# Optimization experiments

Measured on AMD Instinct MI355X. Metric: run time of the kernel, lower is better.

## Reference

```python
import jax, jax.numpy as jnp
import numpy as np

T, B, S = 64, 32, 128
E, Q, H = 512, 512, 256  # src_encoding_size, query_vec_size, hidden_dim


def setup_inputs() -> dict:
    key = jax.random.key(0)
    ks = jax.random.split(key, 9)
    return {
        "src_encodings": jax.random.normal(ks[0], (B, S, E), jnp.float32),
        "src_token_mask": jax.random.randint(ks[1], (B, S), 0, 2).astype(bool),
        "query_vec": jax.random.normal(ks[2], (T, B, Q), jnp.float32),
        # learned params (nn.Linear stores W as (out, in))
        "W_src": jax.random.normal(ks[3], (H, E), jnp.float32) * (1.0 / np.sqrt(E)),
        "b_src": jax.random.normal(ks[4], (H,), jnp.float32) * 0.01,
        "W_q": jax.random.normal(ks[5], (H, Q), jnp.float32) * (1.0 / np.sqrt(Q)),
        "b_q": jax.random.normal(ks[6], (H,), jnp.float32) * 0.01,
        "w2": jax.random.normal(ks[7], (H,), jnp.float32) * (1.0 / np.sqrt(H)),
        "b2": jax.random.normal(ks[8], (), jnp.float32) * 0.01,
    }


def reference(src_encodings, src_token_mask, query_vec, W_src, b_src, W_q, b_q, w2, b2):
    # src projection: (B,S,H); query projection: (T,B,H)
    src_proj = jnp.einsum('bse,he->bsh', src_encodings, W_src) + b_src
    q_proj = jnp.einsum('tbq,hq->tbh', query_vec, W_q) + b_q
    # broadcast add -> tanh: (T,B,S,H)
    h1 = jnp.tanh(src_proj[None, :, :, :] + q_proj[:, :, None, :])
    # hidden -> 1 reduction: (T,B,S)
    h2 = jnp.einsum('tbsh,h->tbs', h1, w2) + b2
    h2 = jnp.where(src_token_mask[None, :, :], -jnp.inf, h2)
    return jax.nn.softmax(h2, axis=-1)
```

## Files before the change

### kernel.cpp

```cpp
#include <hip/hip_runtime.h>
#include <hip/hip_bf16.h>
#include <math.h>


#define TANH_PRESCALE 2.8853900817779268f
#define LOG2E        1.4426950408889634f

typedef __attribute__((ext_vector_type(8))) short short8;
typedef __attribute__((ext_vector_type(4))) float f32x4;

__device__ __forceinline__ float fast_exp2(float x) {
#if __has_builtin(__builtin_amdgcn_exp2f)
    return __builtin_amdgcn_exp2f(x);
#else
    return exp2f(x);
#endif
}
__device__ __forceinline__ float fast_rcp(float x) {
#if __has_builtin(__builtin_amdgcn_rcpf)
    return __builtin_amdgcn_rcpf(x);
#else
    return 1.0f / x;
#endif
}
__device__ __forceinline__ float hi_part(float x) {
    return __uint_as_float(__float_as_uint(x) & 0xffff0000u);
}
__device__ __forceinline__ unsigned pack2(float a, float b) {
    return __builtin_amdgcn_perm(__float_as_uint(b), __float_as_uint(a), 0x07060302u);
}

#define AHI 0
#define ALO 4608
#define WHI 9216
#define WLO 13824
#define LDS_USH 18432

__global__ __launch_bounds__(256) void proj_gemm(
    const float* __restrict__ src, const float* __restrict__ query,
    const float* __restrict__ Wsrc, const float* __restrict__ Wq,
    const float* __restrict__ b_src, const float* __restrict__ b_q,
    float* __restrict__ spq, float* __restrict__ qp)
{
    const int lin = blockIdx.x;
    const int g   = lin & 7;
    const int r   = lin >> 3;
    const int nb  = r & 3;
    const int bx  = (r >> 2) * 8 + g;

    const bool isSrc = bx < 64;
    const int mrow0 = (isSrc ? bx : bx - 64) * 64;
    const float* __restrict__ A    = isSrc ? src  : query;
    const float* __restrict__ W    = isSrc ? Wsrc : Wq;
    const float* __restrict__ bias = isSrc ? b_src : b_q;

    __shared__ unsigned short LS[LDS_USH];

    const int tid  = threadIdx.x;
    const int lane = tid & 63;
    const int wv   = tid >> 6;
    const int wm   = wv & 1, wn = wv >> 1;
    const int l15  = lane & 15;
    const int q4   = lane >> 4;

    const int srow = tid >> 3;
    const int sc8  = tid & 7;

    f32x4 acc[2][2];
    #pragma unroll
    for (int i = 0; i < 2; ++i)
        #pragma unroll
        for (int j = 0; j < 2; ++j) acc[i][j] = (f32x4){0.f, 0.f, 0.f, 0.f};

    const float* Ab = A + (size_t)mrow0 * 512 + sc8 * 8;
    const float* Wb = W + (size_t)(nb * 64) * 512 + sc8 * 8;

    for (int kt = 0; kt < 512; kt += 64) {
        __syncthreads();
        #pragma unroll
        for (int p = 0; p < 2; ++p) {
            const int row = srow + 32 * p;
            const float* gp = Ab + (size_t)row * 512 + kt;
            float4 v0 = *(const float4*)gp, v1 = *(const float4*)(gp + 4);
            uint4 h; uint4 l;
            h.x = pack2(v0.x, v0.y);  h.y = pack2(v0.z, v0.w);
            h.z = pack2(v1.x, v1.y);  h.w = pack2(v1.z, v1.w);
            l.x = pack2(v0.x - hi_part(v0.x), v0.y - hi_part(v0.y));
            l.y = pack2(v0.z - hi_part(v0.z), v0.w - hi_part(v0.w));
            l.z = pack2(v1.x - hi_part(v1.x), v1.y - hi_part(v1.y));
            l.w = pack2(v1.z - hi_part(v1.z), v1.w - hi_part(v1.w));
            *(uint4*)&LS[AHI + row * 72 + sc8 * 8] = h;
            *(uint4*)&LS[ALO + row * 72 + sc8 * 8] = l;
        }
        #pragma unroll
        for (int p = 0; p < 2; ++p) {
            const int row = srow + 32 * p;
            const float* gp = Wb + (size_t)row * 512 + kt;
            float4 v0 = *(const float4*)gp, v1 = *(const float4*)(gp + 4);
            uint4 h; uint4 l;
            h.x = pack2(v0.x, v0.y);  h.y = pack2(v0.z, v0.w);
            h.z = pack2(v1.x, v1.y);  h.w = pack2(v1.z, v1.w);
            l.x = pack2(v0.x - hi_part(v0.x), v0.y - hi_part(v0.y));
            l.y = pack2(v0.z - hi_part(v0.z), v0.w - hi_part(v0.w));
            l.z = pack2(v1.x - hi_part(v1.x), v1.y - hi_part(v1.y));
            l.w = pack2(v1.z - hi_part(v1.z), v1.w - hi_part(v1.w));
            *(uint4*)&LS[WHI + row * 72 + sc8 * 8] = h;
            *(uint4*)&LS[WLO + row * 72 + sc8 * 8] = l;
        }
        __syncthreads();

        #pragma unroll
        for (int pass = 0; pass < 3; ++pass) {
            const unsigned short* Ap = LS + (pass == 2 ? ALO : AHI);
            const unsigned short* Wp = LS + (pass == 1 ? WLO : WHI);
            #pragma unroll
            for (int kk = 0; kk < 2; ++kk) {
                const int off = (kk * 4 + q4) * 8;
                short8 a0 = *(const short8*)&Ap[(wm * 32 + l15)      * 72 + off];
                short8 a1 = *(const short8*)&Ap[(wm * 32 + 16 + l15) * 72 + off];
                short8 w0 = *(const short8*)&Wp[(wn * 32 + l15)      * 72 + off];
                short8 w1 = *(const short8*)&Wp[(wn * 32 + 16 + l15) * 72 + off];
                acc[0][0] = __builtin_amdgcn_mfma_f32_16x16x32_bf16(a0, w0, acc[0][0], 0, 0, 0);
                acc[0][1] = __builtin_amdgcn_mfma_f32_16x16x32_bf16(a0, w1, acc[0][1], 0, 0, 0);
                acc[1][0] = __builtin_amdgcn_mfma_f32_16x16x32_bf16(a1, w0, acc[1][0], 0, 0, 0);
                acc[1][1] = __builtin_amdgcn_mfma_f32_16x16x32_bf16(a1, w1, acc[1][1], 0, 0, 0);
            }
        }
    }

    float bl[2];
    #pragma unroll
    for (int ni = 0; ni < 2; ++ni)
        bl[ni] = bias[nb * 64 + wn * 32 + ni * 16 + l15];

    __syncthreads();
    float* E = (float*)LS;
    #pragma unroll
    for (int mi = 0; mi < 2; ++mi)
        #pragma unroll
        for (int ni = 0; ni < 2; ++ni) {
            const int m = wm * 32 + mi * 16 + q4 * 4;
            const int n = wn * 32 + ni * 16 + l15;
            #pragma unroll
            for (int rr = 0; rr < 4; ++rr)
                E[(m + rr) * 68 + n] = (acc[mi][ni][rr] + bl[ni]) * TANH_PRESCALE;
        }
    __syncthreads();

    if (isSrc) {
        const int nq = tid >> 4;
        #pragma unroll
        for (int j = 0; j < 4; ++j) {
            const int m = (tid & 15) + 16 * j;
            float4 v = *(const float4*)&E[m * 68 + nq * 4];
            *(float4*)(spq + (size_t)(nb * 16 + nq) * 16384
                           + (size_t)(mrow0 + m) * 4) = v;
        }
    } else {
        #pragma unroll
        for (int p = 0; p < 4; ++p) {
            const int idx = p * 256 + tid;
            const int m = idx >> 4, c4 = idx & 15;
            float4 v = *(const float4*)&E[m * 68 + c4 * 4];
            *(float4*)(qp + (size_t)(mrow0 + m) * 256 + nb * 64 + c4 * 4) = v;
        }
    }
}

__global__ __launch_bounds__(512) void attn_score(
    const float* __restrict__ spq, const float* __restrict__ qp,
    const float* __restrict__ w2, const int* __restrict__ mask,
    float* __restrict__ out)
{
    const int lin = blockIdx.x;
    const int gx  = lin & 7;
    const int rr  = lin >> 3;
    const int tz  = rr & 15;
    const int b   = (rr >> 4) * 8 + gx;

    const int tid = threadIdx.x;

    __shared__ float qp_s[4][256];
    __shared__ float w2_s[256];
    __shared__ float h2p[4][4][128];

    int mk0 = 0, mk1 = 0;
    if (tid < 256) {
        const int tl = tid >> 6, lane = tid & 63;
        const int t = tz * 4 + tl;
        *(float4*)&qp_s[tl][lane * 4] =
            *(const float4*)(qp + (size_t)(t * 32 + b) * 256 + lane * 4);
        mk0 = mask[b * 128 + lane];
        mk1 = mask[b * 128 + lane + 64];
    } else if (tid < 320) {
        const int i = tid - 256;
        *(float4*)&w2_s[i * 4] = *(const float4*)(w2 + i * 4);
    }
    __syncthreads();

    const int s = tid & 127;
    const int g4 = tid >> 7;
    const int hb = g4 * 64;
    const float* sq = spq + (size_t)(g4 * 16) * 16384 + (size_t)(b * 128 + s) * 4;

    float acc0 = 0.f, acc1 = 0.f, acc2 = 0.f, acc3 = 0.f;
    float4 s4 = *(const float4*)sq;
    #pragma unroll 4
    for (int hq = 0; hq < 16; ++hq) {
        float4 nxt;
        if (hq < 15) nxt = *(const float4*)(sq + (size_t)(hq + 1) * 16384);
        float4 w4 = *(const float4*)&w2_s[hb + hq * 4];
        float4 q0 = *(const float4*)&qp_s[0][hb + hq * 4];
        float4 q1 = *(const float4*)&qp_s[1][hb + hq * 4];
        float4 q2 = *(const float4*)&qp_s[2][hb + hq * 4];
        float4 q3 = *(const float4*)&qp_s[3][hb + hq * 4];
        #define PN_TERM(sj, wj, q0j, q1j, q2j, q3j)                              \
            { float r_;                                                          \
              r_ = fast_rcp(fast_exp2(sj + q0j) + 1.0f); acc0 = fmaf(wj, r_, acc0);\
              r_ = fast_rcp(fast_exp2(sj + q1j) + 1.0f); acc1 = fmaf(wj, r_, acc1);\
              r_ = fast_rcp(fast_exp2(sj + q2j) + 1.0f); acc2 = fmaf(wj, r_, acc2);\
              r_ = fast_rcp(fast_exp2(sj + q3j) + 1.0f); acc3 = fmaf(wj, r_, acc3); }
        PN_TERM(s4.x, w4.x, q0.x, q1.x, q2.x, q3.x)
        PN_TERM(s4.y, w4.y, q0.y, q1.y, q2.y, q3.y)
        PN_TERM(s4.z, w4.z, q0.z, q1.z, q2.z, q3.z)
        PN_TERM(s4.w, w4.w, q0.w, q1.w, q2.w, q3.w)
        #undef PN_TERM
        s4 = nxt;
    }
    h2p[g4][0][s] = acc0;
    h2p[g4][1][s] = acc1;
    h2p[g4][2][s] = acc2;
    h2p[g4][3][s] = acc3;
    __syncthreads();

    if (tid < 256) {
        const int wv = tid >> 6, lane = tid & 63;
        float v0 = -2.0f * (h2p[0][wv][lane] + h2p[1][wv][lane]
                          + h2p[2][wv][lane] + h2p[3][wv][lane]);
        float v1 = -2.0f * (h2p[0][wv][lane + 64] + h2p[1][wv][lane + 64]
                          + h2p[2][wv][lane + 64] + h2p[3][wv][lane + 64]);
        if (mk0) v0 = -__builtin_inff();
        if (mk1) v1 = -__builtin_inff();

        float mx = fmaxf(v0, v1);
        #pragma unroll
        for (int off = 32; off >= 1; off >>= 1) mx = fmaxf(mx, __shfl_xor(mx, off));
        float e0 = fast_exp2((v0 - mx) * LOG2E);
        float e1 = fast_exp2((v1 - mx) * LOG2E);
        float sum = e0 + e1;
        #pragma unroll
        for (int off = 32; off >= 1; off >>= 1) sum += __shfl_xor(sum, off);
        const float r_ = fast_rcp(sum);

        const size_t ob = (size_t)((tz * 4 + wv) * 32 + b) * 128;
        out[ob + lane]      = e0 * r_;
        out[ob + lane + 64] = e1 * r_;
    }
}

extern "C" void kernel_launch(void* const* d_in, const int* in_sizes, int n_in,
                              void* d_out, int out_size, void* d_ws, size_t ws_size,
                              hipStream_t stream) {
    const float* src   = (const float*)d_in[0];
    const int*   mask  = (const int*)  d_in[1];
    const float* query = (const float*)d_in[2];
    const float* W_src = (const float*)d_in[3];
    const float* b_src = (const float*)d_in[4];
    const float* W_q   = (const float*)d_in[5];
    const float* b_q   = (const float*)d_in[6];
    const float* w2    = (const float*)d_in[7];
    float* out = (float*)d_out;

    float* spq = (float*)d_ws;
    float* qp  = (float*)((char*)d_ws + (4u << 20));

    proj_gemm<<<384, 256, 0, stream>>>(src, query, W_src, W_q,
                                       b_src, b_q, spq, qp);
    attn_score<<<512, 512, 0, stream>>>(spq, qp, w2, mask, out);
}
```

Measured before the change: 102.2 us.

## Stage src projections through double-buffered LDS and simplify block index mapping

The attention-score kernel now prefetches the src-projection chunks from global memory into a double-buffered shared-memory tile and computes from that tile. Previously each thread streamed its own chunks straight from global memory. Both kernels also drop the XCD-aware block swizzle in favour of plain grid indexing, with proj_gemm launched on a 2D grid. The change adds two block barriers per stage and more LDS use. Removing the swizzle may also hurt L2 locality across the chiplets.

```diff
diff --git a/kernel.cpp b/kernel.cpp
--- a/kernel.cpp
+++ b/kernel.cpp
@@ -42,12 +42,8 @@
     const float* __restrict__ b_src, const float* __restrict__ b_q,
     float* __restrict__ spq, float* __restrict__ qp)
 {
-    const int lin = blockIdx.x;
-    const int g   = lin & 7;
-    const int r   = lin >> 3;
-    const int nb  = r & 3;
-    const int bx  = (r >> 2) * 8 + g;
-
+    const int bx = blockIdx.x;
+    const int nb = blockIdx.y;
     const bool isSrc = bx < 64;
     const int mrow0 = (isSrc ? bx : bx - 64) * 64;
     const float* __restrict__ A    = isSrc ? src  : query;
@@ -173,16 +169,15 @@
     float* __restrict__ out)
 {
     const int lin = blockIdx.x;
-    const int gx  = lin & 7;
-    const int rr  = lin >> 3;
-    const int tz  = rr & 15;
-    const int b   = (rr >> 4) * 8 + gx;
+    const int b   = lin & 31;
+    const int tz  = lin >> 5;
 
     const int tid = threadIdx.x;
 
-    __shared__ float qp_s[4][256];
-    __shared__ float w2_s[256];
-    __shared__ float h2p[4][4][128];
+    __shared__ float4 spq_s[2][8][128];
+    __shared__ float  qp_s[4][256];
+    __shared__ float  w2_s[256];
+    __shared__ float  h2p[4][4][128];
 
     int mk0 = 0, mk1 = 0;
     if (tid < 256) {
@@ -196,37 +191,65 @@
         const int i = tid - 256;
         *(float4*)&w2_s[i * 4] = *(const float4*)(w2 + i * 4);
     }
+
+    const int slot0 = tid >> 7;
+    const int slot1 = 4 + (tid >> 7);
+    const int s_i   = tid & 127;
+    const float* sp_b = spq + (size_t)(b * 128 + s_i) * 4;
+    #define GHQ(q, p) (((q) >> 1) * 16 + (p) * 2 + ((q) & 1))
+    #define GLOAD(q, p) (*(const float4*)(sp_b + (size_t)GHQ(q, p) * 16384))
+
+    {
+        float4 r0 = GLOAD(slot0, 0);
+        float4 r1 = GLOAD(slot1, 0);
+        spq_s[0][slot0][s_i] = r0;
+        spq_s[0][slot1][s_i] = r1;
+    }
     __syncthreads();
 
-    const int s = tid & 127;
+    const int s  = tid & 127;
     const int g4 = tid >> 7;
     const int hb = g4 * 64;
-    const float* sq = spq + (size_t)(g4 * 16) * 16384 + (size_t)(b * 128 + s) * 4;
 
     float acc0 = 0.f, acc1 = 0.f, acc2 = 0.f, acc3 = 0.f;
-    float4 s4 = *(const float4*)sq;
-    #pragma unroll 4
-    for (int hq = 0; hq < 16; ++hq) {
-        float4 nxt;
-        if (hq < 15) nxt = *(const float4*)(sq + (size_t)(hq + 1) * 16384);
-        float4 w4 = *(const float4*)&w2_s[hb + hq * 4];
-        float4 q0 = *(const float4*)&qp_s[0][hb + hq * 4];
-        float4 q1 = *(const float4*)&qp_s[1][hb + hq * 4];
-        float4 q2 = *(const float4*)&qp_s[2][hb + hq * 4];
-        float4 q3 = *(const float4*)&qp_s[3][hb + hq * 4];
-        #define PN_TERM(sj, wj, q0j, q1j, q2j, q3j)                              \
-            { float r_;                                                          \
-              r_ = fast_rcp(fast_exp2(sj + q0j) + 1.0f); acc0 = fmaf(wj, r_, acc0);\
-              r_ = fast_rcp(fast_exp2(sj + q1j) + 1.0f); acc1 = fmaf(wj, r_, acc1);\
-              r_ = fast_rcp(fast_exp2(sj + q2j) + 1.0f); acc2 = fmaf(wj, r_, acc2);\
-              r_ = fast_rcp(fast_exp2(sj + q3j) + 1.0f); acc3 = fmaf(wj, r_, acc3); }
-        PN_TERM(s4.x, w4.x, q0.x, q1.x, q2.x, q3.x)
-        PN_TERM(s4.y, w4.y, q0.y, q1.y, q2.y, q3.y)
-        PN_TERM(s4.z, w4.z, q0.z, q1.z, q2.z, q3.z)
-        PN_TERM(s4.w, w4.w, q0.w, q1.w, q2.w, q3.w)
-        #undef PN_TERM
-        s4 = nxt;
-    }
+
+    #pragma unroll
+    for (int p = 0; p < 8; ++p) {
+        float4 r0, r1;
+        if (p < 7) {
+            r0 = GLOAD(slot0, p + 1);
+            r1 = GLOAD(slot1, p + 1);
+        }
+        const int buf = p & 1;
+        #pragma unroll
+        for (int k = 0; k < 2; ++k) {
+            const int hq = p * 2 + k;
+            float4 s4 = spq_s[buf][g4 * 2 + k][s];
+            float4 w4 = *(const float4*)&w2_s[hb + hq * 4];
+            float4 q0 = *(const float4*)&qp_s[0][hb + hq * 4];
+            float4 q1 = *(const float4*)&qp_s[1][hb + hq * 4];
+            float4 q2 = *(const float4*)&qp_s[2][hb + hq * 4];
+            float4 q3 = *(const float4*)&qp_s[3][hb + hq * 4];
+            #define PN_TERM(sj, wj, q0j, q1j, q2j, q3j)                              \
+                { float r_;                                                          \
+                  r_ = fast_rcp(fast_exp2(sj + q0j) + 1.0f); acc0 = fmaf(wj, r_, acc0);\
+                  r_ = fast_rcp(fast_exp2(sj + q1j) + 1.0f); acc1 = fmaf(wj, r_, acc1);\
+                  r_ = fast_rcp(fast_exp2(sj + q2j) + 1.0f); acc2 = fmaf(wj, r_, acc2);\
+                  r_ = fast_rcp(fast_exp2(sj + q3j) + 1.0f); acc3 = fmaf(wj, r_, acc3); }
+            PN_TERM(s4.x, w4.x, q0.x, q1.x, q2.x, q3.x)
+            PN_TERM(s4.y, w4.y, q0.y, q1.y, q2.y, q3.y)
+            PN_TERM(s4.z, w4.z, q0.z, q1.z, q2.z, q3.z)
+            PN_TERM(s4.w, w4.w, q0.w, q1.w, q2.w, q3.w)
+            #undef PN_TERM
+        }
+        if (p < 7) {
+            __syncthreads();
+            spq_s[buf ^ 1][slot0][s_i] = r0;
+            spq_s[buf ^ 1][slot1][s_i] = r1;
+            __syncthreads();
+        }
+    }
+
     h2p[g4][0][s] = acc0;
     h2p[g4][1][s] = acc1;
     h2p[g4][2][s] = acc2;
@@ -274,7 +297,7 @@
     float* spq = (float*)d_ws;
     float* qp  = (float*)((char*)d_ws + (4u << 20));
 
-    proj_gemm<<<384, 256, 0, stream>>>(src, query, W_src, W_q,
-                                       b_src, b_q, spq, qp);
+    proj_gemm<<<dim3(96, 4), 256, 0, stream>>>(src, query, W_src, W_q,
+                                               b_src, b_q, spq, qp);
     attn_score<<<512, 512, 0, stream>>>(spq, qp, w2, mask, out);
 }
```

After: 101.9 us. About the same (-0.3%).
